# Kernel optimization log

Measured on AMD Instinct MI355X. Metric: run time of the kernel, lower is better.

## Reference

```python
import jax, jax.numpy as jnp
import numpy as np

IIR_LEN = 16384
EPS = 1e-5


def causal_fft_conv(x, h):
    # x: (N, L), h: (N, K); causal linear convolution, truncated to length L
    L = x.shape[-1]
    K = h.shape[-1]
    n = L + K
    X = jnp.fft.rfft(x, n)
    H = jnp.fft.rfft(h, n)
    return jnp.fft.irfft(X * H, n)[..., :L]


def setup_inputs() -> dict:
    key = jax.random.key(0)
    k1, k2, k3, k4, k5 = jax.random.split(key, 5)
    return {
        "input_signals": jax.random.normal(k1, (32, 2, 131072), dtype=jnp.float32),
        "z_alpha": jax.random.normal(k2, (32, 1), dtype=jnp.float32),
        "log_threshold": jax.random.normal(k3, (32, 1), dtype=jnp.float32),
        "log_ratio": jax.random.normal(k4, (32, 1), dtype=jnp.float32),
        "log_knee": jax.random.normal(k5, (32, 1), dtype=jnp.float32),
    }


def reference(input_signals, z_alpha, log_threshold, log_ratio, log_knee):
    # --- IIR envelope follower approximated by a long FIR (FFT conv) ---
    alpha = jax.nn.sigmoid(z_alpha)                          # (N, 1)
    arange = jnp.arange(IIR_LEN, dtype=input_signals.dtype)  # (K,)
    # h_env[n] = (1 - alpha) * alpha**n, computed stably in log domain
    h = (1.0 - alpha) * jnp.exp(arange[None, :] * jnp.log(alpha))  # (N, K)
    energy = jnp.mean(jnp.square(input_signals), axis=1)           # (N, L)
    envelope = causal_fft_conv(energy, h)                          # (N, L)
    log_energy = jnp.log(envelope + EPS)                           # G_u

    # --- quadratic-knee gain computer (gain = G_y - G_u) ---
    T = log_threshold - 6.0            # (N, 1)
    R = 1.0 + jnp.exp(log_ratio)       # ratio in [1, inf)
    W = jnp.exp(log_knee)              # knee width
    c = 1.0 / R - 1.0
    above = log_energy >= T + W
    below = log_energy < T - W
    g_above = c * (log_energy - T)
    g_mid = c * jnp.square(log_energy - T + W) / (4.0 * W)
    log_gain = jnp.where(above, g_above, jnp.where(below, 0.0, g_mid))

    gain = jnp.exp(log_gain)                       # (N, L)
    return gain[:, None, :] * input_signals        # (N, C, L)
```

## Files before the change

kernel.cpp:

```cpp
#include <hip/hip_runtime.h>
#include <math.h>


namespace {

constexpr int N_BATCH = 32;
constexpr int L_LEN   = 131072;
constexpr int NCHUNK  = 64;
constexpr int CL      = L_LEN / NCHUNK;
constexpr int NTHR    = 256;
constexpr int SEG     = CL / NTHR;
constexpr int NWAVE   = NTHR / 64;
constexpr int NBLK    = NCHUNK * N_BATCH;
constexpr int NXCD    = 8;
constexpr float EPS_F = 1e-5f;
constexpr float LOG2E = 1.4426950408889634f;

__device__ __forceinline__ float fast_exp2(float x) {
#if __has_builtin(__builtin_amdgcn_exp2f)
    return __builtin_amdgcn_exp2f(x);
#else
    return exp2f(x);
#endif
}
__device__ __forceinline__ float fast_log2(float x) {
#if __has_builtin(__builtin_amdgcn_logf)
    return __builtin_amdgcn_logf(x);
#else
    return log2f(x);
#endif
}

__device__ __forceinline__ void batch_alpha(float z, float& alpha, float& oma, float& la2) {
    if (z >= 0.f) {
        float e = expf(-z);
        float d = 1.f + e;
        alpha = 1.f / d;
        oma   = e / d;
        la2   = -log1pf(e) * LOG2E;
    } else {
        float e = expf(z);
        float d = 1.f + e;
        alpha = e / d;
        oma   = 1.f / d;
        la2   = (z - log1pf(e)) * LOG2E;
    }
}

__global__ __launch_bounds__(NTHR, 4) void k_compress(
    const float* __restrict__ x,
    const float* __restrict__ z_alpha,
    const float* __restrict__ log_threshold,
    const float* __restrict__ log_ratio,
    const float* __restrict__ log_knee,
    float* __restrict__ out)
{
    const int bid  = blockIdx.x;
    const int work = (bid & (NXCD - 1)) * (NBLK / NXCD) + (bid >> 3);
    const int n    = work >> 6;
    const int c    = work & (NCHUNK - 1);
    const int t    = threadIdx.x;
    const int lane = t & 63;
    const int wv   = t >> 6;

    const size_t base = (size_t)n * 2 * L_LEN + (size_t)c * CL + (size_t)t * SEG;
    const float* x0 = x + base;
    const float* x1 = x0 + L_LEN;

    float4 a0 = *reinterpret_cast<const float4*>(x0);
    float4 a1 = *reinterpret_cast<const float4*>(x0 + 4);
    float4 b0 = *reinterpret_cast<const float4*>(x1);
    float4 b1 = *reinterpret_cast<const float4*>(x1 + 4);

    float alpha, oma, la2;
    batch_alpha(z_alpha[n], alpha, oma, la2);
    const float h_oma = 0.5f * oma;

    __shared__ float part[NWAVE];
    __shared__ float wA[NWAVE], wB[NWAVE];

    const float wexp = (float)(SEG * (NTHR - 1 - t)) * la2;
    float v = 0.f;
    if (c > 0 && wexp > -126.f) {
        const float* p0 = x0 - CL;
        const float* p1 = p0 + L_LEN;
        float4 pa0 = *reinterpret_cast<const float4*>(p0);
        float4 pa1 = *reinterpret_cast<const float4*>(p0 + 4);
        float4 pb0 = *reinterpret_cast<const float4*>(p1);
        float4 pb1 = *reinterpret_cast<const float4*>(p1 + 4);
        float yl = 0.f;
        yl = fmaf(alpha, yl, h_oma * fmaf(pa0.x, pa0.x, pb0.x * pb0.x));
        yl = fmaf(alpha, yl, h_oma * fmaf(pa0.y, pa0.y, pb0.y * pb0.y));
        yl = fmaf(alpha, yl, h_oma * fmaf(pa0.z, pa0.z, pb0.z * pb0.z));
        yl = fmaf(alpha, yl, h_oma * fmaf(pa0.w, pa0.w, pb0.w * pb0.w));
        yl = fmaf(alpha, yl, h_oma * fmaf(pa1.x, pa1.x, pb1.x * pb1.x));
        yl = fmaf(alpha, yl, h_oma * fmaf(pa1.y, pa1.y, pb1.y * pb1.y));
        yl = fmaf(alpha, yl, h_oma * fmaf(pa1.z, pa1.z, pb1.z * pb1.z));
        yl = fmaf(alpha, yl, h_oma * fmaf(pa1.w, pa1.w, pb1.w * pb1.w));
        v = fast_exp2(wexp) * yl;
    }
    #pragma unroll
    for (int d = 32; d > 0; d >>= 1) v += __shfl_down(v, d);
    if (lane == 0) part[wv] = v;

    float e[SEG];
    e[0] = fmaf(a0.x, a0.x, b0.x * b0.x);
    e[1] = fmaf(a0.y, a0.y, b0.y * b0.y);
    e[2] = fmaf(a0.z, a0.z, b0.z * b0.z);
    e[3] = fmaf(a0.w, a0.w, b0.w * b0.w);
    e[4] = fmaf(a1.x, a1.x, b1.x * b1.x);
    e[5] = fmaf(a1.y, a1.y, b1.y * b1.y);
    e[6] = fmaf(a1.z, a1.z, b1.z * b1.z);
    e[7] = fmaf(a1.w, a1.w, b1.w * b1.w);

    float f = 0.f;
    #pragma unroll
    for (int i = 0; i < SEG; ++i) f = fmaf(alpha, f, h_oma * e[i]);

    float A = fast_exp2((float)SEG * la2);
    float b = f;
    #pragma unroll
    for (int d = 1; d < 64; d <<= 1) {
        float Ap = __shfl_up(A, d);
        float bp = __shfl_up(b, d);
        if (lane >= d) {
            b = fmaf(A, bp, b);
            A *= Ap;
        }
    }
    if (lane == 63) { wA[wv] = A; wB[wv] = b; }

    __syncthreads();

    float carry = 0.f;
    if (c > 0) {
        #pragma unroll
        for (int k = 0; k < NWAVE; ++k) carry += part[k];
    }

    float PA = 1.f, PB = 0.f;
    #pragma unroll
    for (int k = 0; k < NWAVE - 1; ++k) {
        if (k < wv) {
            PB = fmaf(wA[k], PB, wB[k]);
            PA *= wA[k];
        }
    }
    float EA = __shfl_up(A, 1);
    float EB = __shfl_up(b, 1);
    if (lane == 0) { EA = 1.f; EB = 0.f; }
    float y = fmaf(EA, fmaf(PA, carry, PB), EB);

    const float T2    = (log_threshold[n] - 6.0f) * LOG2E;
    const float R     = 1.0f + expf(log_ratio[n]);
    const float cc    = 1.0f / R - 1.0f;
    const float W2    = expf(log_knee[n]) * LOG2E;
    const float i4W2  = 1.0f / (4.0f * W2);

    float gn[SEG];
    #pragma unroll
    for (int i = 0; i < SEG; ++i) {
        y = fmaf(alpha, y, h_oma * e[i]);
        float le2 = fast_log2(y + EPS_F);
        float g2;
        if (le2 >= T2 + W2) {
            g2 = cc * (le2 - T2);
        } else if (le2 < T2 - W2) {
            g2 = 0.f;
        } else {
            float u = le2 - T2 + W2;
            g2 = cc * u * u * i4W2;
        }
        gn[i] = fast_exp2(g2);
    }

    float* o0 = out + base;
    float* o1 = o0 + L_LEN;
    *reinterpret_cast<float4*>(o0)     = make_float4(gn[0]*a0.x, gn[1]*a0.y, gn[2]*a0.z, gn[3]*a0.w);
    *reinterpret_cast<float4*>(o0 + 4) = make_float4(gn[4]*a1.x, gn[5]*a1.y, gn[6]*a1.z, gn[7]*a1.w);
    *reinterpret_cast<float4*>(o1)     = make_float4(gn[0]*b0.x, gn[1]*b0.y, gn[2]*b0.z, gn[3]*b0.w);
    *reinterpret_cast<float4*>(o1 + 4) = make_float4(gn[4]*b1.x, gn[5]*b1.y, gn[6]*b1.z, gn[7]*b1.w);
}

}

extern "C" void kernel_launch(void* const* d_in, const int* in_sizes, int n_in,
                              void* d_out, int out_size, void* d_ws, size_t ws_size,
                              hipStream_t stream) {
    const float* x  = (const float*)d_in[0];
    const float* za = (const float*)d_in[1];
    const float* lt = (const float*)d_in[2];
    const float* lr = (const float*)d_in[3];
    const float* lk = (const float*)d_in[4];
    float* out = (float*)d_out;

    k_compress<<<NBLK, NTHR, 0, stream>>>(x, za, lt, lr, lk, out);
}
```

Baseline: 19.91 us.

## Make each wave an independent chunk to remove block-level shared-memory sync

Shrinks the chunk size from a block-wide 2048 samples to a per-wave 512 samples, so each wave computes its own carry from the preceding chunk via a wave-level xor reduction. This drops the shared-memory partials, the cross-wave prefix combine and the __syncthreads barrier. In exchange every wave re-reads its predecessor chunk's lookback window, which means more redundant loads and exp2 work per output. The launch-bounds occupancy hint is also removed.

```diff
diff --git a/kernel.cpp b/kernel.cpp
--- a/kernel.cpp
+++ b/kernel.cpp
@@ -6,12 +6,13 @@
 
 constexpr int N_BATCH = 32;
 constexpr int L_LEN   = 131072;
-constexpr int NCHUNK  = 64;
-constexpr int CL      = L_LEN / NCHUNK;
 constexpr int NTHR    = 256;
-constexpr int SEG     = CL / NTHR;
+constexpr int SEG     = 8;
+constexpr int WCHUNK  = 64 * SEG;
 constexpr int NWAVE   = NTHR / 64;
-constexpr int NBLK    = NCHUNK * N_BATCH;
+constexpr int CPB     = N_BATCH * L_LEN / WCHUNK;
+constexpr int NBLK    = CPB / NWAVE;
+constexpr int BPB     = L_LEN / (WCHUNK * NWAVE);
 constexpr int NXCD    = 8;
 constexpr float EPS_F = 1e-5f;
 constexpr float LOG2E = 1.4426950408889634f;
@@ -47,7 +48,7 @@
     }
 }
 
-__global__ __launch_bounds__(NTHR, 4) void k_compress(
+__global__ __launch_bounds__(NTHR) void k_compress(
     const float* __restrict__ x,
     const float* __restrict__ z_alpha,
     const float* __restrict__ log_threshold,
@@ -57,13 +58,12 @@
 {
     const int bid  = blockIdx.x;
     const int work = (bid & (NXCD - 1)) * (NBLK / NXCD) + (bid >> 3);
-    const int n    = work >> 6;
-    const int c    = work & (NCHUNK - 1);
-    const int t    = threadIdx.x;
-    const int lane = t & 63;
-    const int wv   = t >> 6;
+    const int n    = work / BPB;
+    const int wv   = (threadIdx.x >> 6);
+    const int c    = (work % BPB) * NWAVE + wv;
+    const int lane = threadIdx.x & 63;
 
-    const size_t base = (size_t)n * 2 * L_LEN + (size_t)c * CL + (size_t)t * SEG;
+    const size_t base = (size_t)n * 2 * L_LEN + (size_t)c * WCHUNK + (size_t)lane * SEG;
     const float* x0 = x + base;
     const float* x1 = x0 + L_LEN;
 
@@ -76,13 +76,10 @@
     batch_alpha(z_alpha[n], alpha, oma, la2);
     const float h_oma = 0.5f * oma;
 
-    __shared__ float part[NWAVE];
-    __shared__ float wA[NWAVE], wB[NWAVE];
-
-    const float wexp = (float)(SEG * (NTHR - 1 - t)) * la2;
+    const float wexp = (float)(SEG * (63 - lane)) * la2;
     float v = 0.f;
     if (c > 0 && wexp > -126.f) {
-        const float* p0 = x0 - CL;
+        const float* p0 = x0 - WCHUNK;
         const float* p1 = p0 + L_LEN;
         float4 pa0 = *reinterpret_cast<const float4*>(p0);
         float4 pa1 = *reinterpret_cast<const float4*>(p0 + 4);
@@ -100,22 +97,18 @@
         v = fast_exp2(wexp) * yl;
     }
     #pragma unroll
-    for (int d = 32; d > 0; d >>= 1) v += __shfl_down(v, d);
-    if (lane == 0) part[wv] = v;
-
-    float e[SEG];
-    e[0] = fmaf(a0.x, a0.x, b0.x * b0.x);
-    e[1] = fmaf(a0.y, a0.y, b0.y * b0.y);
-    e[2] = fmaf(a0.z, a0.z, b0.z * b0.z);
-    e[3] = fmaf(a0.w, a0.w, b0.w * b0.w);
-    e[4] = fmaf(a1.x, a1.x, b1.x * b1.x);
-    e[5] = fmaf(a1.y, a1.y, b1.y * b1.y);
-    e[6] = fmaf(a1.z, a1.z, b1.z * b1.z);
-    e[7] = fmaf(a1.w, a1.w, b1.w * b1.w);
+    for (int d = 1; d < 64; d <<= 1) v += __shfl_xor(v, d);
+    const float carry = v;
 
     float f = 0.f;
-    #pragma unroll
-    for (int i = 0; i < SEG; ++i) f = fmaf(alpha, f, h_oma * e[i]);
+    f = fmaf(alpha, f, h_oma * fmaf(a0.x, a0.x, b0.x * b0.x));
+    f = fmaf(alpha, f, h_oma * fmaf(a0.y, a0.y, b0.y * b0.y));
+    f = fmaf(alpha, f, h_oma * fmaf(a0.z, a0.z, b0.z * b0.z));
+    f = fmaf(alpha, f, h_oma * fmaf(a0.w, a0.w, b0.w * b0.w));
+    f = fmaf(alpha, f, h_oma * fmaf(a1.x, a1.x, b1.x * b1.x));
+    f = fmaf(alpha, f, h_oma * fmaf(a1.y, a1.y, b1.y * b1.y));
+    f = fmaf(alpha, f, h_oma * fmaf(a1.z, a1.z, b1.z * b1.z));
+    f = fmaf(alpha, f, h_oma * fmaf(a1.w, a1.w, b1.w * b1.w));
 
     float A = fast_exp2((float)SEG * la2);
     float b = f;
@@ -128,36 +121,28 @@
             A *= Ap;
         }
     }
-    if (lane == 63) { wA[wv] = A; wB[wv] = b; }
 
-    __syncthreads();
-
-    float carry = 0.f;
-    if (c > 0) {
-        #pragma unroll
-        for (int k = 0; k < NWAVE; ++k) carry += part[k];
-    }
-
-    float PA = 1.f, PB = 0.f;
-    #pragma unroll
-    for (int k = 0; k < NWAVE - 1; ++k) {
-        if (k < wv) {
-            PB = fmaf(wA[k], PB, wB[k]);
-            PA *= wA[k];
-        }
-    }
     float EA = __shfl_up(A, 1);
     float EB = __shfl_up(b, 1);
     if (lane == 0) { EA = 1.f; EB = 0.f; }
-    float y = fmaf(EA, fmaf(PA, carry, PB), EB);
+    float y = fmaf(EA, carry, EB);
 
-    const float T2    = (log_threshold[n] - 6.0f) * LOG2E;
-    const float R     = 1.0f + expf(log_ratio[n]);
-    const float cc    = 1.0f / R - 1.0f;
-    const float W2    = expf(log_knee[n]) * LOG2E;
-    const float i4W2  = 1.0f / (4.0f * W2);
+    const float T2   = (log_threshold[n] - 6.0f) * LOG2E;
+    const float R    = 1.0f + expf(log_ratio[n]);
+    const float cc   = 1.0f / R - 1.0f;
+    const float W2   = expf(log_knee[n]) * LOG2E;
+    const float i4W2 = 1.0f / (4.0f * W2);
 
     float gn[SEG];
+    float e[SEG];
+    e[0] = fmaf(a0.x, a0.x, b0.x * b0.x);
+    e[1] = fmaf(a0.y, a0.y, b0.y * b0.y);
+    e[2] = fmaf(a0.z, a0.z, b0.z * b0.z);
+    e[3] = fmaf(a0.w, a0.w, b0.w * b0.w);
+    e[4] = fmaf(a1.x, a1.x, b1.x * b1.x);
+    e[5] = fmaf(a1.y, a1.y, b1.y * b1.y);
+    e[6] = fmaf(a1.z, a1.z, b1.z * b1.z);
+    e[7] = fmaf(a1.w, a1.w, b1.w * b1.w);
     #pragma unroll
     for (int i = 0; i < SEG; ++i) {
         y = fmaf(alpha, y, h_oma * e[i]);
```

Result: faster. 18.28 us (-8.2%).
